# Optimization experiments

Hardware: AMD Instinct MI355X
Metric: run time of the kernel (lower is better)

## Reference

```python
import jax, jax.numpy as jnp
import numpy as np
from jax import lax

N_QUANTIZE = 256
N_AUX = 28
N_RESCH = 512
N_SKIPCH = 256
KS = 2
DILATIONS = [2 ** i for i in range(10)] * 3  # 30 layers
L = len(DILATIONS)


def _causal_conv(x, w, b, d):
    # x: (B, Cin, T), w: (Cout, Cin, KS) torch Conv1d layout, left-pad => causal
    pad = (w.shape[-1] - 1) * d
    y = lax.conv_general_dilated(x, w, window_strides=(1,), padding=[(pad, 0)],
                                 rhs_dilation=(d,),
                                 dimension_numbers=('NCH', 'OIH', 'NCH'))
    return y + b[None, :, None]


def _conv1x1(x, w, b):
    # x: (B, Cin, T), w: (Cout, Cin)
    return jnp.einsum('oi,bit->bot', w, x) + b[None, :, None]


def setup_inputs() -> dict:
    key = jax.random.key(0)
    ks = jax.random.split(key, 20)
    B, T = 2, 8000
    s = 0.05
    rn = lambda k, shape: (jax.random.normal(k, shape, jnp.float32) * s)
    inp = {
        'x': jax.random.randint(ks[0], (B, T), 0, N_QUANTIZE),
        'h': jax.random.normal(ks[1], (B, N_AUX, T), jnp.float32),
        'causal_w': rn(ks[2], (N_RESCH, N_QUANTIZE, KS)),
        'causal_b': rn(ks[3], (N_RESCH,)),
        'dil_sig_w': rn(ks[4], (L, N_RESCH, N_RESCH, KS)),
        'dil_sig_b': rn(ks[5], (L, N_RESCH)),
        'dil_tanh_w': rn(ks[6], (L, N_RESCH, N_RESCH, KS)),
        'dil_tanh_b': rn(ks[7], (L, N_RESCH)),
        'aux_sig_w': rn(ks[8], (L, N_RESCH, N_AUX)),
        'aux_sig_b': rn(ks[9], (L, N_RESCH)),
        'aux_tanh_w': rn(ks[10], (L, N_RESCH, N_AUX)),
        'aux_tanh_b': rn(ks[11], (L, N_RESCH)),
        'skip_w': rn(ks[12], (L, N_SKIPCH, N_RESCH)),
        'skip_b': rn(ks[13], (L, N_SKIPCH)),
        'res_w': rn(ks[14], (L, N_RESCH, N_RESCH)),
        'res_b': rn(ks[15], (L, N_RESCH)),
        'post1_w': rn(ks[16], (N_SKIPCH, N_SKIPCH)),
        'post1_b': rn(ks[17], (N_SKIPCH,)),
        'post2_w': rn(ks[18], (N_QUANTIZE, N_SKIPCH)),
        'post2_b': rn(ks[19], (N_QUANTIZE,)),
    }
    return inp


def reference(x, h, causal_w, causal_b, dil_sig_w, dil_sig_b, dil_tanh_w, dil_tanh_b,
              aux_sig_w, aux_sig_b, aux_tanh_w, aux_tanh_b, skip_w, skip_b,
              res_w, res_b, post1_w, post1_b, post2_w, post2_b):
    B, T = x.shape
    # _preprocess: onehot (B,T,Q) -> (B,Q,T), then causal conv
    oh = jax.nn.one_hot(x % N_QUANTIZE, N_QUANTIZE, dtype=jnp.float32).transpose(0, 2, 1)
    out = _causal_conv(oh, causal_w, causal_b, 1)  # (B, n_resch, T)
    skip_sum = jnp.zeros((B, N_SKIPCH, T), jnp.float32)
    for l, d in enumerate(DILATIONS):
        sig = _causal_conv(out, dil_sig_w[l], dil_sig_b[l], d) + _conv1x1(h, aux_sig_w[l], aux_sig_b[l])
        tan = _causal_conv(out, dil_tanh_w[l], dil_tanh_b[l], d) + _conv1x1(h, aux_tanh_w[l], aux_tanh_b[l])
        z = jax.nn.sigmoid(sig) * jnp.tanh(tan)
        skip_sum = skip_sum + _conv1x1(z, skip_w[l], skip_b[l])
        out = _conv1x1(z, res_w[l], res_b[l]) + out
    # _postprocess: relu -> 1x1 -> relu -> 1x1 -> (B, T, n_quantize)
    y = jax.nn.relu(skip_sum)
    y = jax.nn.relu(_conv1x1(y, post1_w, post1_b))
    y = _conv1x1(y, post2_w, post2_b)
    return y.transpose(0, 2, 1)
```

## Files before the change

kernel.cpp:

```cpp
#include <hip/hip_runtime.h>
#include <math.h>

#define T_LEN 8000
#define BATCH 2
#define CCH 512
#define SKP 256
#define AUXP 32
#define NQ 256
#define NLAYER 30
#define PADF 512
#define TPAD 8192
#define ROWS (PADF + TPAD)
#define HROWS TPAD

typedef unsigned short hfu;
typedef unsigned int u32;
typedef __attribute__((ext_vector_type(8))) _Float16 half8;
typedef __attribute__((ext_vector_type(4))) float f32x4;

#define GLOAD16(g, l)                                                          \
  __builtin_amdgcn_global_load_lds(                                            \
      (const __attribute__((address_space(1))) void*)(g),                      \
      (__attribute__((address_space(3))) void*)(l), 16, 0, 0)

__device__ inline hfu hfbits(float f) {
  union { _Float16 h; hfu u; } x;
  x.h = (_Float16)f;
  return x.u;
}
__device__ inline u32 pk2(float a, float b) {
  return (u32)hfbits(a) | ((u32)hfbits(b) << 16);
}
__device__ inline uint4 pk8(const float f[8]) {
  return make_uint4(pk2(f[0], f[1]), pk2(f[2], f[3]), pk2(f[4], f[5]), pk2(f[6], f[7]));
}
__device__ inline int ldsL(int row, int ck) {
  return ((row >> 1) << 3) + ((((ck) ^ ((row >> 1) & 3)) << 1) | (row & 1));
}

__global__ __launch_bounds__(256) void zero16(uint4* p, int n) {
  for (int i = blockIdx.x * 256 + threadIdx.x; i < n; i += gridDim.x * 256)
    p[i] = make_uint4(0u, 0u, 0u, 0u);
}

__global__ __launch_bounds__(256) void cvt_dil(const float* __restrict__ in, hfu* __restrict__ out) {
  const long NG = (long)NLAYER * CCH * (CCH / 4);
  for (long g = (long)blockIdx.x * 256 + threadIdx.x; g < NG; g += (long)gridDim.x * 256) {
    const int i4 = (int)(g & 127) * 4;
    const int o = (int)((g >> 7) & 511);
    const int l = (int)(g >> 16);
    const float* pp = in + (((size_t)l * CCH + o) * CCH + i4) * 2;
    float4 f0 = *(const float4*)pp;
    float4 f1 = *(const float4*)(pp + 4);
    uint2 t0 = make_uint2(pk2(f0.x, f0.z), pk2(f1.x, f1.z));
    uint2 t1 = make_uint2(pk2(f0.y, f0.w), pk2(f1.y, f1.w));
    hfu* ob = out + ((size_t)l * 2 * CCH + o) * CCH + i4;
    *(uint2*)ob = t0;
    *(uint2*)(ob + (size_t)CCH * CCH) = t1;
  }
}

__global__ __launch_bounds__(256) void cvt_skipres(const float* __restrict__ skw,
                                                   const float* __restrict__ rsw,
                                                   hfu* __restrict__ out) {
  const long NG = (long)NLAYER * 768 * (CCH / 4);
  for (long g = (long)blockIdx.x * 256 + threadIdx.x; g < NG; g += (long)gridDim.x * 256) {
    const int i4 = (int)(g & 127) * 4;
    const int r = (int)((g >> 7) % 768);
    const int l = (int)(g / (128 * 768));
    const float* src = (r < SKP) ? (skw + ((size_t)l * SKP + r) * CCH + i4)
                                 : (rsw + ((size_t)l * CCH + (r - SKP)) * CCH + i4);
    float4 f = *(const float4*)src;
    *(uint2*)(out + ((size_t)l * 768 + r) * CCH + i4) = make_uint2(pk2(f.x, f.y), pk2(f.z, f.w));
  }
}

__global__ __launch_bounds__(256) void cvt_aux(const float* __restrict__ in, hfu* __restrict__ out) {
  const int N = NLAYER * CCH * AUXP;
  for (int i = blockIdx.x * 256 + threadIdx.x; i < N; i += gridDim.x * 256) {
    const int j = i & 31;
    const int o = (i >> 5) & 511;
    const int l = i >> 14;
    float v = (j < 28) ? in[((size_t)l * CCH + o) * 28 + j] : 0.f;
    out[i] = hfbits(v);
  }
}

__global__ __launch_bounds__(256) void cvt_copy(const float* __restrict__ in, hfu* __restrict__ out, int n) {
  for (int i = blockIdx.x * 256 + threadIdx.x; i < n; i += gridDim.x * 256)
    out[i] = hfbits(in[i]);
}

__global__ __launch_bounds__(256) void cvt_cwt(const float* __restrict__ cw, float* __restrict__ out) {
  const int N = 2 * NQ * CCH;
  for (int i = blockIdx.x * 256 + threadIdx.x; i < N; i += gridDim.x * 256) {
    const int tap = i >> 17;
    const int r = i & 131071;
    const int xq = r >> 9;
    const int o = r & 511;
    out[i] = cw[((size_t)o * NQ + xq) * 2 + tap];
  }
}

__global__ __launch_bounds__(256) void htrans_kernel(const float* __restrict__ h, hfu* __restrict__ hbf) {
  const int b = blockIdx.y;
  const int t = blockIdx.x * 64 + (threadIdx.x & 63);
  const int j0 = threadIdx.x >> 6;
#pragma unroll
  for (int j = j0; j < AUXP; j += 4) {
    float v = (j < 28 && t < T_LEN) ? h[((size_t)b * 28 + j) * T_LEN + t] : 0.f;
    hbf[((size_t)b * HROWS + t) * AUXP + j] = hfbits(v);
  }
}

template <int PRE>
__global__ __launch_bounds__(256) void embed_kernel(const int* __restrict__ x,
                                                    const float* __restrict__ cwt,
                                                    const float* __restrict__ cb,
                                                    float* __restrict__ outf,
                                                    hfu* __restrict__ outb) {
  const int b = blockIdx.y;
  const int t = blockIdx.x * 4 + (threadIdx.x >> 6);
  const int o = (threadIdx.x & 63) * 8;
  const int xc = x[(size_t)b * T_LEN + t] & 255;
  const int xp = (t > 0) ? (x[(size_t)b * T_LEN + t - 1] & 255) : 0;
  const float won = (t > 0) ? 1.f : 0.f;
  const float* c1 = cwt + 131072 + (size_t)xc * CCH + o;
  const float* c0 = cwt + (size_t)xp * CCH + o;
  float v[8];
#pragma unroll
  for (int j = 0; j < 8; ++j) v[j] = cb[o + j] + c1[j] + won * c0[j];
  if (PRE) {
    *(uint4*)&outb[((size_t)b * ROWS + PADF + t) * CCH + o] = pk8(v);
  } else {
    float* po = outf + ((size_t)b * ROWS + PADF + t) * CCH + o;
    *(float4*)po = make_float4(v[0], v[1], v[2], v[3]);
    *(float4*)(po + 4) = make_float4(v[4], v[5], v[6], v[7]);
  }
}

template <int PRE>
__global__ __launch_bounds__(512, 2) void gate_kernel(
    const hfu* __restrict__ actb, const float* __restrict__ actf,
    const hfu* __restrict__ hbf,
    const void* __restrict__ wsp, const void* __restrict__ wtp,
    const hfu* __restrict__ auxs, const hfu* __restrict__ auxt,
    const float* __restrict__ bs1, const float* __restrict__ bs2,
    const float* __restrict__ bt1, const float* __restrict__ bt2,
    hfu* __restrict__ z, int d) {
  __shared__ uint4 sm[4096];
  const int tid = threadIdx.x;
  const int lane = tid & 63, wid = tid >> 6;
  const int wm = wid >> 2, wn = wid & 3;
  const int lr = lane & 15, lq = lane >> 4;

  const int n = blockIdx.x;
  const int f = (n & 7) * 32 + (n >> 3);
  const int tt = f >> 3, inner = f & 7;
  const int o0 = (inner >> 1) * 128;
  const int b = inner & 1;
  const int t0 = tt * 256;

  f32x4 accS[4][4] = {};
  f32x4 accT[4][4] = {};

  auto stage = [&](int ih, int p) {
    const int base = p * 2048;
    const int pr = tid >> 3, w = tid & 7;
    const int row = (pr << 1) | (w & 1);
    const int ck = (w >> 1) ^ (pr & 3);
    if (ih < 32) {
      const int tau = (ih < 16) ? 1 : 0;
      const int koff = (ih & 15) * 32;
      if (PRE) {
        const size_t wo = ((size_t)tau * CCH + o0 + row) * CCH + koff + ck * 8;
        GLOAD16((const hfu*)wsp + wo, &sm[base + tid]);
        GLOAD16((const hfu*)wtp + wo, &sm[base + 512 + tid]);
#pragma unroll
        for (int c = 0; c < 2; ++c) {
          const int s = c * 512 + tid;
          const int pr2 = s >> 3, w2 = s & 7;
          const int row2 = (pr2 << 1) | (w2 & 1);
          const int ck2 = (w2 >> 1) ^ (pr2 & 3);
          const hfu* ar = actb + ((size_t)b * ROWS + PADF + t0 + row2 - (tau ? 0 : d)) * CCH + koff + ck2 * 8;
          GLOAD16(ar, &sm[base + 1024 + s]);
        }
      } else {
        const float* wsf = (const float*)wsp;
        const float* wtf = (const float*)wtp;
        const size_t fb = ((size_t)(o0 + row) * CCH + koff + ck * 8) * 2;
        float vs[8], vt[8];
#pragma unroll
        for (int j = 0; j < 4; ++j) {
          float4 fs = *(const float4*)&wsf[fb + j * 4];
          float4 ft = *(const float4*)&wtf[fb + j * 4];
          vs[2 * j] = tau ? fs.y : fs.x;
          vs[2 * j + 1] = tau ? fs.w : fs.z;
          vt[2 * j] = tau ? ft.y : ft.x;
          vt[2 * j + 1] = tau ? ft.w : ft.z;
        }
        sm[base + tid] = pk8(vs);
        sm[base + 512 + tid] = pk8(vt);
#pragma unroll
        for (int c = 0; c < 2; ++c) {
          const int s = c * 512 + tid;
          const int pr2 = s >> 3, w2 = s & 7;
          const int row2 = (pr2 << 1) | (w2 & 1);
          const int ck2 = (w2 >> 1) ^ (pr2 & 3);
          const float* ar = actf + ((size_t)b * ROWS + PADF + t0 + row2 - (tau ? 0 : d)) * CCH + koff + ck2 * 8;
          float4 f0 = *(const float4*)&ar[0];
          float4 f1 = *(const float4*)&ar[4];
          float vb[8] = {f0.x, f0.y, f0.z, f0.w, f1.x, f1.y, f1.z, f1.w};
          sm[base + 1024 + s] = pk8(vb);
        }
      }
    } else {
      if (PRE) {
        GLOAD16(auxs + (size_t)(o0 + row) * AUXP + ck * 8, &sm[base + tid]);
        GLOAD16(auxt + (size_t)(o0 + row) * AUXP + ck * 8, &sm[base + 512 + tid]);
      } else {
        sm[base + tid] = *(const uint4*)&auxs[(size_t)(o0 + row) * AUXP + ck * 8];
        sm[base + 512 + tid] = *(const uint4*)&auxt[(size_t)(o0 + row) * AUXP + ck * 8];
      }
#pragma unroll
      for (int c = 0; c < 2; ++c) {
        const int s = c * 512 + tid;
        const int pr2 = s >> 3, w2 = s & 7;
        const int row2 = (pr2 << 1) | (w2 & 1);
        const int ck2 = (w2 >> 1) ^ (pr2 & 3);
        if (PRE)
          GLOAD16(hbf + ((size_t)b * HROWS + t0 + row2) * AUXP + ck2 * 8, &sm[base + 1024 + s]);
        else
          sm[base + 1024 + s] = *(const uint4*)&hbf[((size_t)b * HROWS + t0 + row2) * AUXP + ck2 * 8];
      }
    }
  };

  auto compute = [&](int p) {
    const int base = p * 2048;
    half8 af[4], ag[4], bv[4];
#pragma unroll
    for (int mr = 0; mr < 4; ++mr) {
      const int row = wm * 64 + mr * 16 + lr;
      const int idx = ldsL(row, lq);
      af[mr] = *(const half8*)&sm[base + idx];
      ag[mr] = *(const half8*)&sm[base + 512 + idx];
    }
#pragma unroll
    for (int nr = 0; nr < 4; ++nr) {
      const int row = wn * 64 + nr * 16 + lr;
      bv[nr] = *(const half8*)&sm[base + 1024 + ldsL(row, lq)];
    }
#pragma unroll
    for (int mr = 0; mr < 4; ++mr)
#pragma unroll
      for (int nr = 0; nr < 4; ++nr) {
        accS[mr][nr] = __builtin_amdgcn_mfma_f32_16x16x32_f16(af[mr], bv[nr], accS[mr][nr], 0, 0, 0);
        accT[mr][nr] = __builtin_amdgcn_mfma_f32_16x16x32_f16(ag[mr], bv[nr], accT[mr][nr], 0, 0, 0);
      }
  };

  if (PRE) {
    stage(0, 0);
    for (int ih = 0; ih < 33; ++ih) {
      if (ih < 32) {
        stage(ih + 1, (ih + 1) & 1);
        asm volatile("s_waitcnt vmcnt(4)" ::: "memory");
      } else {
        asm volatile("s_waitcnt vmcnt(0)" ::: "memory");
      }
      __builtin_amdgcn_s_barrier();
      __builtin_amdgcn_sched_barrier(0);
      __builtin_amdgcn_s_setprio(1);
      compute(ih & 1);
      __builtin_amdgcn_s_setprio(0);
      __builtin_amdgcn_sched_barrier(0);
      __builtin_amdgcn_s_barrier();
    }
  } else {
    for (int ih = 0; ih < 33; ++ih) {
      stage(ih, ih & 1);
      __syncthreads();
      compute(ih & 1);
      __syncthreads();
    }
  }

#pragma unroll
  for (int mr = 0; mr < 4; ++mr) {
    const int ob = o0 + wm * 64 + mr * 16 + lq * 4;
    float4 x1 = *(const float4*)&bs1[ob];
    float4 x2 = *(const float4*)&bs2[ob];
    float4 y1 = *(const float4*)&bt1[ob];
    float4 y2 = *(const float4*)&bt2[ob];
    const float sb[4] = {x1.x + x2.x, x1.y + x2.y, x1.z + x2.z, x1.w + x2.w};
    const float tb[4] = {y1.x + y2.x, y1.y + y2.y, y1.z + y2.z, y1.w + y2.w};
#pragma unroll
    for (int nr = 0; nr < 4; ++nr) {
      const int t = t0 + wn * 64 + nr * 16 + lr;
      float zv[4];
#pragma unroll
      for (int j = 0; j < 4; ++j) {
        float sv = accS[mr][nr][j] + sb[j];
        float tv = accT[mr][nr][j] + tb[j];
        float sg = __builtin_amdgcn_rcpf(1.f + __expf(-sv));
        float e2 = __expf(2.f * tv);
        float th = 1.f - 2.f * __builtin_amdgcn_rcpf(e2 + 1.f);
        zv[j] = sg * th;
      }
      *(uint2*)&z[((size_t)b * HROWS + t) * CCH + ob] = make_uint2(pk2(zv[0], zv[1]), pk2(zv[2], zv[3]));
    }
  }
}

template <int PRE>
__global__ __launch_bounds__(512, 4) void update_kernel(
    const hfu* __restrict__ z, const void* __restrict__ wp,
    const float* __restrict__ skwf, const float* __restrict__ rswf,
    const float* __restrict__ skb, const float* __restrict__ rsb,
    float* __restrict__ skip, float* __restrict__ outf, hfu* __restrict__ outb) {
  __shared__ uint4 sm[2048];
  const int tid = threadIdx.x;
  const int lane = tid & 63, wid = tid >> 6;
  const int wm = wid >> 1, wn = wid & 1;
  const int lr = lane & 15, lq = lane >> 4;

  const int n = blockIdx.x;
  const int xcd = n & 7, j = n >> 3;
  const int ttl = j / 12, inner = j % 12;
  const int tt = xcd * 8 + ttl;
  if (tt > 62) return;
  const int rg = inner >> 1, b = inner & 1;
  const int r0 = rg * 128;
  const int t0 = tt * 128;

  f32x4 acc[2][4] = {};

  auto stage_u = [&](int ih, int p) {
    const int base = p * 1024;
    const int pr = tid >> 3, w = tid & 7;
    const int row = (pr << 1) | (w & 1);
    const int ck = (w >> 1) ^ (pr & 3);
    const int k0 = ih * 32;
    if (PRE) {
      GLOAD16((const hfu*)wp + (size_t)(r0 + row) * CCH + k0 + ck * 8, &sm[base + tid]);
      GLOAD16(z + ((size_t)b * HROWS + t0 + row) * CCH + k0 + ck * 8, &sm[base + 512 + tid]);
    } else {
      const int R = r0 + row;
      const float* src = (R < SKP) ? (skwf + (size_t)R * CCH + k0 + ck * 8)
                                   : (rswf + (size_t)(R - SKP) * CCH + k0 + ck * 8);
      float4 f0 = *(const float4*)&src[0];
      float4 f1 = *(const float4*)&src[4];
      float v[8] = {f0.x, f0.y, f0.z, f0.w, f1.x, f1.y, f1.z, f1.w};
      sm[base + tid] = pk8(v);
      sm[base + 512 + tid] = *(const uint4*)&z[((size_t)b * HROWS + t0 + row) * CCH + k0 + ck * 8];
    }
  };

  auto compute_u = [&](int p) {
    const int base = p * 1024;
    half8 av[2], bv[4];
#pragma unroll
    for (int mr = 0; mr < 2; ++mr) {
      const int row = wm * 32 + mr * 16 + lr;
      av[mr] = *(const half8*)&sm[base + ldsL(row, lq)];
    }
#pragma unroll
    for (int nr = 0; nr < 4; ++nr) {
      const int row = wn * 64 + nr * 16 + lr;
      bv[nr] = *(const half8*)&sm[base + 512 + ldsL(row, lq)];
    }
#pragma unroll
    for (int mr = 0; mr < 2; ++mr)
#pragma unroll
      for (int nr = 0; nr < 4; ++nr)
        acc[mr][nr] = __builtin_amdgcn_mfma_f32_16x16x32_f16(av[mr], bv[nr], acc[mr][nr], 0, 0, 0);
  };

  if (PRE) {
    stage_u(0, 0);
    for (int ih = 0; ih < 16; ++ih) {
      if (ih < 15) {
        stage_u(ih + 1, (ih + 1) & 1);
        asm volatile("s_waitcnt vmcnt(2)" ::: "memory");
      } else {
        asm volatile("s_waitcnt vmcnt(0)" ::: "memory");
      }
      __builtin_amdgcn_s_barrier();
      __builtin_amdgcn_sched_barrier(0);
      __builtin_amdgcn_s_setprio(1);
      compute_u(ih & 1);
      __builtin_amdgcn_s_setprio(0);
      __builtin_amdgcn_sched_barrier(0);
      __builtin_amdgcn_s_barrier();
    }
  } else {
    for (int ih = 0; ih < 16; ++ih) {
      stage_u(ih, ih & 1);
      __syncthreads();
      compute_u(ih & 1);
      __syncthreads();
    }
  }

  const bool iskip = (r0 < SKP);
#pragma unroll
  for (int mr = 0; mr < 2; ++mr) {
    const int R = r0 + wm * 32 + mr * 16 + lq * 4;
#pragma unroll
    for (int nr = 0; nr < 4; ++nr) {
      const int t = t0 + wn * 64 + nr * 16 + lr;
      if (t < T_LEN) {
        if (iskip) {
          float4 bb = *(const float4*)&skb[R];
          float4* p = (float4*)&skip[((size_t)b * T_LEN + t) * SKP + R];
          float4 v = *p;
          v.x += acc[mr][nr][0] + bb.x;
          v.y += acc[mr][nr][1] + bb.y;
          v.z += acc[mr][nr][2] + bb.z;
          v.w += acc[mr][nr][3] + bb.w;
          *p = v;
        } else {
          const int rr = R - SKP;
          float4 bb = *(const float4*)&rsb[rr];
          if (PRE) {
            hfu* pb = &outb[((size_t)b * ROWS + PADF + t) * CCH + rr];
            uint2 old = *(uint2*)pb;
            const _Float16* hp = (const _Float16*)&old;
            float v0 = (float)hp[0] + acc[mr][nr][0] + bb.x;
            float v1 = (float)hp[1] + acc[mr][nr][1] + bb.y;
            float v2 = (float)hp[2] + acc[mr][nr][2] + bb.z;
            float v3 = (float)hp[3] + acc[mr][nr][3] + bb.w;
            *(uint2*)pb = make_uint2(pk2(v0, v1), pk2(v2, v3));
          } else {
            float4* p = (float4*)&outf[((size_t)b * ROWS + PADF + t) * CCH + rr];
            float4 v = *p;
            v.x += acc[mr][nr][0] + bb.x;
            v.y += acc[mr][nr][1] + bb.y;
            v.z += acc[mr][nr][2] + bb.z;
            v.w += acc[mr][nr][3] + bb.w;
            *p = v;
          }
        }
      }
    }
  }
}

__global__ __launch_bounds__(256, 2) void post1_kernel(const float* __restrict__ skip,
                                                       const hfu* __restrict__ w,
                                                       const float* __restrict__ bias,
                                                       hfu* __restrict__ y1) {
  __shared__ uint4 sm[2048];
  uint4* sA = sm;
  uint4* sB = sm + 1024;
  const int tid = threadIdx.x;
  const int lane = tid & 63, wid = tid >> 6;
  const int wm = wid >> 1, wn = wid & 1;
  const int lr = lane & 15, lq = lane >> 4;
  const int t0 = blockIdx.x * 128;
  const int r0 = blockIdx.y * 128;
  const int b = blockIdx.z;
  f32x4 acc[4][4] = {};
  for (int kt = 0; kt < 4; ++kt) {
#pragma unroll
    for (int c = 0; c < 4; ++c) {
      const int cb = c * 256 + wid * 64;
      const int ch = cb + lane;
      const int ksub = ch >> 7, mn = ch & 127;
      const int k0 = kt * 64 + ksub * 8;
      GLOAD16(w + (size_t)(r0 + mn) * SKP + k0, &sA[cb]);
      int row = t0 + mn;
      if (row > T_LEN - 1) row = T_LEN - 1;
      const float* src = skip + ((size_t)b * T_LEN + row) * SKP + k0;
      float4 f0 = *(const float4*)&src[0];
      float4 f1 = *(const float4*)&src[4];
      float v[8] = {fmaxf(f0.x, 0.f), fmaxf(f0.y, 0.f), fmaxf(f0.z, 0.f), fmaxf(f0.w, 0.f),
                    fmaxf(f1.x, 0.f), fmaxf(f1.y, 0.f), fmaxf(f1.z, 0.f), fmaxf(f1.w, 0.f)};
      sB[ch] = pk8(v);
    }
    __syncthreads();
#pragma unroll
    for (int ks = 0; ks < 2; ++ks) {
      const int kb = (ks * 4 + lq) * 128;
      half8 av[4], bv[4];
#pragma unroll
      for (int r = 0; r < 4; ++r) {
        av[r] = *(const half8*)&sA[kb + wm * 64 + r * 16 + lr];
        bv[r] = *(const half8*)&sB[kb + wn * 64 + r * 16 + lr];
      }
#pragma unroll
      for (int mr = 0; mr < 4; ++mr)
#pragma unroll
        for (int nr = 0; nr < 4; ++nr)
          acc[mr][nr] = __builtin_amdgcn_mfma_f32_16x16x32_f16(av[mr], bv[nr], acc[mr][nr], 0, 0, 0);
    }
    __syncthreads();
  }
#pragma unroll
  for (int mr = 0; mr < 4; ++mr) {
    const int ob = r0 + wm * 64 + mr * 16 + lq * 4;
    float4 bb = *(const float4*)&bias[ob];
    const float bs[4] = {bb.x, bb.y, bb.z, bb.w};
#pragma unroll
    for (int nr = 0; nr < 4; ++nr) {
      const int t = t0 + wn * 64 + nr * 16 + lr;
      float v[4];
#pragma unroll
      for (int j = 0; j < 4; ++j) v[j] = fmaxf(acc[mr][nr][j] + bs[j], 0.f);
      *(uint2*)&y1[((size_t)b * HROWS + t) * SKP + ob] = make_uint2(pk2(v[0], v[1]), pk2(v[2], v[3]));
    }
  }
}

__global__ __launch_bounds__(256, 2) void post2_kernel(const hfu* __restrict__ y1,
                                                       const hfu* __restrict__ w,
                                                       const float* __restrict__ bias,
                                                       float* __restrict__ outp) {
  __shared__ uint4 sm[2048];
  uint4* sA = sm;
  uint4* sB = sm + 1024;
  const int tid = threadIdx.x;
  const int lane = tid & 63, wid = tid >> 6;
  const int wm = wid >> 1, wn = wid & 1;
  const int lr = lane & 15, lq = lane >> 4;
  const int t0 = blockIdx.x * 128;
  const int r0 = blockIdx.y * 128;
  const int b = blockIdx.z;
  f32x4 acc[4][4] = {};
  for (int kt = 0; kt < 4; ++kt) {
#pragma unroll
    for (int c = 0; c < 4; ++c) {
      const int cb = c * 256 + wid * 64;
      const int ch = cb + lane;
      const int ksub = ch >> 7, mn = ch & 127;
      const int k0 = kt * 64 + ksub * 8;
      GLOAD16(w + (size_t)(r0 + mn) * SKP + k0, &sA[cb]);
      GLOAD16(y1 + ((size_t)b * HROWS + t0 + mn) * SKP + k0, &sB[cb]);
    }
    __syncthreads();
#pragma unroll
    for (int ks = 0; ks < 2; ++ks) {
      const int kb = (ks * 4 + lq) * 128;
      half8 av[4], bv[4];
#pragma unroll
      for (int r = 0; r < 4; ++r) {
        av[r] = *(const half8*)&sA[kb + wm * 64 + r * 16 + lr];
        bv[r] = *(const half8*)&sB[kb + wn * 64 + r * 16 + lr];
      }
#pragma unroll
      for (int mr = 0; mr < 4; ++mr)
#pragma unroll
        for (int nr = 0; nr < 4; ++nr)
          acc[mr][nr] = __builtin_amdgcn_mfma_f32_16x16x32_f16(av[mr], bv[nr], acc[mr][nr], 0, 0, 0);
    }
    __syncthreads();
  }
#pragma unroll
  for (int mr = 0; mr < 4; ++mr) {
    const int ob = r0 + wm * 64 + mr * 16 + lq * 4;
    float4 bb = *(const float4*)&bias[ob];
#pragma unroll
    for (int nr = 0; nr < 4; ++nr) {
      const int t = t0 + wn * 64 + nr * 16 + lr;
      if (t < T_LEN) {
        float4 v;
        v.x = acc[mr][nr][0] + bb.x;
        v.y = acc[mr][nr][1] + bb.y;
        v.z = acc[mr][nr][2] + bb.z;
        v.w = acc[mr][nr][3] + bb.w;
        *(float4*)&outp[((size_t)b * T_LEN + t) * NQ + ob] = v;
      }
    }
  }
}

extern "C" void kernel_launch(void* const* d_in, const int* in_sizes, int n_in,
                              void* d_out, int out_size, void* d_ws, size_t ws_size,
                              hipStream_t stream) {
  const int* x = (const int*)d_in[0];
  const float* h = (const float*)d_in[1];
  const float* causal_w = (const float*)d_in[2];
  const float* causal_b = (const float*)d_in[3];
  const float* dil_sig_w = (const float*)d_in[4];
  const float* dil_sig_b = (const float*)d_in[5];
  const float* dil_tanh_w = (const float*)d_in[6];
  const float* dil_tanh_b = (const float*)d_in[7];
  const float* aux_sig_w = (const float*)d_in[8];
  const float* aux_sig_b = (const float*)d_in[9];
  const float* aux_tanh_w = (const float*)d_in[10];
  const float* aux_tanh_b = (const float*)d_in[11];
  const float* skip_w = (const float*)d_in[12];
  const float* skip_b = (const float*)d_in[13];
  const float* res_w = (const float*)d_in[14];
  const float* res_b = (const float*)d_in[15];
  const float* post1_w = (const float*)d_in[16];
  const float* post1_b = (const float*)d_in[17];
  const float* post2_w = (const float*)d_in[18];
  const float* post2_b = (const float*)d_in[19];
  float* outp = (float*)d_out;

  char* p = (char*)d_ws;
  auto alloc = [&](size_t bytes) {
    char* r = p;
    p += (bytes + 255) & ~(size_t)255;
    return r;
  };
  float* outf = (float*)alloc((size_t)BATCH * ROWS * CCH * 4);
  float* skip = (float*)alloc((size_t)BATCH * T_LEN * SKP * 4);
  hfu* zb = (hfu*)alloc((size_t)BATCH * HROWS * CCH * 2);
  hfu* hbf = (hfu*)alloc((size_t)BATCH * HROWS * AUXP * 2);
  hfu* auxsb = (hfu*)alloc((size_t)NLAYER * CCH * AUXP * 2);
  hfu* auxtb = (hfu*)alloc((size_t)NLAYER * CCH * AUXP * 2);
  hfu* p1b = (hfu*)alloc((size_t)NQ * SKP * 2);
  hfu* p2b = (hfu*)alloc((size_t)NQ * SKP * 2);
  float* cwt = (float*)alloc((size_t)2 * NQ * CCH * 4);
  hfu* y1 = zb;
  hfu* outb = (hfu*)alloc((size_t)BATCH * ROWS * CCH * 2);
  hfu* dilS = (hfu*)alloc((size_t)NLAYER * 2 * CCH * CCH * 2);
  hfu* dilT = (hfu*)alloc((size_t)NLAYER * 2 * CCH * CCH * 2);
  hfu* wsr = (hfu*)alloc((size_t)NLAYER * 768 * CCH * 2);
  const bool pre = ((size_t)(p - (char*)d_ws) <= ws_size);

  cvt_aux<<<256, 256, 0, stream>>>(aux_sig_w, auxsb);
  cvt_aux<<<256, 256, 0, stream>>>(aux_tanh_w, auxtb);
  cvt_copy<<<64, 256, 0, stream>>>(post1_w, p1b, NQ * SKP);
  cvt_copy<<<64, 256, 0, stream>>>(post2_w, p2b, NQ * SKP);
  cvt_cwt<<<1024, 256, 0, stream>>>(causal_w, cwt);
  if (pre) {
    cvt_dil<<<2048, 256, 0, stream>>>(dil_sig_w, dilS);
    cvt_dil<<<2048, 256, 0, stream>>>(dil_tanh_w, dilT);
    cvt_skipres<<<2048, 256, 0, stream>>>(skip_w, res_w, wsr);
  }

  zero16<<<512, 256, 0, stream>>>((uint4*)skip, (int)((size_t)BATCH * T_LEN * SKP * 4 / 16));
  for (int b = 0; b < BATCH; ++b) {
    if (pre) {
      zero16<<<32, 256, 0, stream>>>((uint4*)(outb + (size_t)b * ROWS * CCH), PADF * CCH * 2 / 16);
      zero16<<<48, 256, 0, stream>>>((uint4*)(outb + ((size_t)b * ROWS + PADF + T_LEN) * CCH),
                                     (TPAD - T_LEN) * CCH * 2 / 16);
    } else {
      zero16<<<64, 256, 0, stream>>>((uint4*)(outf + (size_t)b * ROWS * CCH), PADF * CCH * 4 / 16);
      zero16<<<96, 256, 0, stream>>>((uint4*)(outf + ((size_t)b * ROWS + PADF + T_LEN) * CCH),
                                     (TPAD - T_LEN) * CCH * 4 / 16);
    }
  }

  htrans_kernel<<<dim3(128, 2), 256, 0, stream>>>(h, hbf);
  if (pre)
    embed_kernel<1><<<dim3(2000, 2), 256, 0, stream>>>(x, cwt, causal_b, nullptr, outb);
  else
    embed_kernel<0><<<dim3(2000, 2), 256, 0, stream>>>(x, cwt, causal_b, outf, nullptr);

  for (int l = 0; l < NLAYER; ++l) {
    const int d = 1 << (l % 10);
    if (pre) {
      gate_kernel<1><<<256, 512, 0, stream>>>(
          outb, nullptr, hbf, dilS + (size_t)l * 2 * CCH * CCH, dilT + (size_t)l * 2 * CCH * CCH,
          auxsb + (size_t)l * CCH * AUXP, auxtb + (size_t)l * CCH * AUXP,
          dil_sig_b + (size_t)l * CCH, aux_sig_b + (size_t)l * CCH,
          dil_tanh_b + (size_t)l * CCH, aux_tanh_b + (size_t)l * CCH, zb, d);
      update_kernel<1><<<768, 512, 0, stream>>>(
          zb, wsr + (size_t)l * 768 * CCH, nullptr, nullptr,
          skip_b + (size_t)l * SKP, res_b + (size_t)l * CCH, skip, nullptr, outb);
    } else {
      gate_kernel<0><<<256, 512, 0, stream>>>(
          nullptr, outf, hbf, dil_sig_w + (size_t)l * CCH * CCH * 2,
          dil_tanh_w + (size_t)l * CCH * CCH * 2,
          auxsb + (size_t)l * CCH * AUXP, auxtb + (size_t)l * CCH * AUXP,
          dil_sig_b + (size_t)l * CCH, aux_sig_b + (size_t)l * CCH,
          dil_tanh_b + (size_t)l * CCH, aux_tanh_b + (size_t)l * CCH, zb, d);
      update_kernel<0><<<768, 512, 0, stream>>>(
          zb, nullptr, skip_w + (size_t)l * SKP * CCH, res_w + (size_t)l * CCH * CCH,
          skip_b + (size_t)l * SKP, res_b + (size_t)l * CCH, skip, outf, nullptr);
    }
  }

  post1_kernel<<<dim3(63, 2, BATCH), 256, 0, stream>>>(skip, p1b, post1_b, y1);
  post2_kernel<<<dim3(63, 2, BATCH), 256, 0, stream>>>(y1, p2b, post2_b, outp);
}
```

Before: 2.166 ms.

## Halve gate tile height and use triple-buffered LDS pipeline in gate/update kernels

The gate kernel tile shrinks from 128 to 64 output channels, so the grid doubles to 512 blocks, accumulator registers halve, and launch bounds allow four blocks per CU. Both gate and update kernels move from a double-buffered to a triple-buffered LDS pipeline with prefetch distance two, dropping the trailing barrier per k-step. The aim is more parallelism and better latency hiding across 256 CUs. In exchange each activation tile is reloaded by twice as many blocks, adding global traffic, and LDS use per block grows.

```diff
diff --git a/kernel.cpp b/kernel.cpp
--- a/kernel.cpp
+++ b/kernel.cpp
@@ -140,7 +140,7 @@
 }
 
 template <int PRE>
-__global__ __launch_bounds__(512, 2) void gate_kernel(
+__global__ __launch_bounds__(512, 4) void gate_kernel(
     const hfu* __restrict__ actb, const float* __restrict__ actf,
     const hfu* __restrict__ hbf,
     const void* __restrict__ wsp, const void* __restrict__ wtp,
@@ -148,111 +148,105 @@
     const float* __restrict__ bs1, const float* __restrict__ bs2,
     const float* __restrict__ bt1, const float* __restrict__ bt2,
     hfu* __restrict__ z, int d) {
-  __shared__ uint4 sm[4096];
+  __shared__ uint4 sm[4608];
   const int tid = threadIdx.x;
   const int lane = tid & 63, wid = tid >> 6;
   const int wm = wid >> 2, wn = wid & 3;
   const int lr = lane & 15, lq = lane >> 4;
 
   const int n = blockIdx.x;
-  const int f = (n & 7) * 32 + (n >> 3);
-  const int tt = f >> 3, inner = f & 7;
-  const int o0 = (inner >> 1) * 128;
+  const int f = (n & 7) * 64 + (n >> 3);
+  const int tt = f >> 4, inner = f & 15;
+  const int o0 = (inner >> 1) * 64;
   const int b = inner & 1;
   const int t0 = tt * 256;
 
-  f32x4 accS[4][4] = {};
-  f32x4 accT[4][4] = {};
+  f32x4 accS[2][4] = {};
+  f32x4 accT[2][4] = {};
 
   auto stage = [&](int ih, int p) {
-    const int base = p * 2048;
-    const int pr = tid >> 3, w = tid & 7;
+    const int base = p * 1536;
+    const int s = tid & 255;
+    const int pr = s >> 3, w = s & 7;
     const int row = (pr << 1) | (w & 1);
     const int ck = (w >> 1) ^ (pr & 3);
     if (ih < 32) {
       const int tau = (ih < 16) ? 1 : 0;
       const int koff = (ih & 15) * 32;
       if (PRE) {
-        const size_t wo = ((size_t)tau * CCH + o0 + row) * CCH + koff + ck * 8;
-        GLOAD16((const hfu*)wsp + wo, &sm[base + tid]);
-        GLOAD16((const hfu*)wtp + wo, &sm[base + 512 + tid]);
+        const hfu* wsel = (tid < 256) ? (const hfu*)wsp : (const hfu*)wtp;
+        GLOAD16(wsel + ((size_t)tau * CCH + o0 + row) * CCH + koff + ck * 8, &sm[base + tid]);
 #pragma unroll
         for (int c = 0; c < 2; ++c) {
-          const int s = c * 512 + tid;
-          const int pr2 = s >> 3, w2 = s & 7;
+          const int s2 = c * 512 + tid;
+          const int pr2 = s2 >> 3, w2 = s2 & 7;
           const int row2 = (pr2 << 1) | (w2 & 1);
           const int ck2 = (w2 >> 1) ^ (pr2 & 3);
           const hfu* ar = actb + ((size_t)b * ROWS + PADF + t0 + row2 - (tau ? 0 : d)) * CCH + koff + ck2 * 8;
-          GLOAD16(ar, &sm[base + 1024 + s]);
+          GLOAD16(ar, &sm[base + 512 + s2]);
         }
       } else {
-        const float* wsf = (const float*)wsp;
-        const float* wtf = (const float*)wtp;
+        const float* wsel = (tid < 256) ? (const float*)wsp : (const float*)wtp;
         const size_t fb = ((size_t)(o0 + row) * CCH + koff + ck * 8) * 2;
-        float vs[8], vt[8];
+        float vs[8];
 #pragma unroll
         for (int j = 0; j < 4; ++j) {
-          float4 fs = *(const float4*)&wsf[fb + j * 4];
-          float4 ft = *(const float4*)&wtf[fb + j * 4];
+          float4 fs = *(const float4*)&wsel[fb + j * 4];
           vs[2 * j] = tau ? fs.y : fs.x;
           vs[2 * j + 1] = tau ? fs.w : fs.z;
-          vt[2 * j] = tau ? ft.y : ft.x;
-          vt[2 * j + 1] = tau ? ft.w : ft.z;
         }
         sm[base + tid] = pk8(vs);
-        sm[base + 512 + tid] = pk8(vt);
 #pragma unroll
         for (int c = 0; c < 2; ++c) {
-          const int s = c * 512 + tid;
-          const int pr2 = s >> 3, w2 = s & 7;
+          const int s2 = c * 512 + tid;
+          const int pr2 = s2 >> 3, w2 = s2 & 7;
           const int row2 = (pr2 << 1) | (w2 & 1);
           const int ck2 = (w2 >> 1) ^ (pr2 & 3);
           const float* ar = actf + ((size_t)b * ROWS + PADF + t0 + row2 - (tau ? 0 : d)) * CCH + koff + ck2 * 8;
           float4 f0 = *(const float4*)&ar[0];
           float4 f1 = *(const float4*)&ar[4];
           float vb[8] = {f0.x, f0.y, f0.z, f0.w, f1.x, f1.y, f1.z, f1.w};
-          sm[base + 1024 + s] = pk8(vb);
+          sm[base + 512 + s2] = pk8(vb);
         }
       }
     } else {
+      const hfu* asel = (tid < 256) ? auxs : auxt;
       if (PRE) {
-        GLOAD16(auxs + (size_t)(o0 + row) * AUXP + ck * 8, &sm[base + tid]);
-        GLOAD16(auxt + (size_t)(o0 + row) * AUXP + ck * 8, &sm[base + 512 + tid]);
+        GLOAD16(asel + (size_t)(o0 + row) * AUXP + ck * 8, &sm[base + tid]);
       } else {
-        sm[base + tid] = *(const uint4*)&auxs[(size_t)(o0 + row) * AUXP + ck * 8];
-        sm[base + 512 + tid] = *(const uint4*)&auxt[(size_t)(o0 + row) * AUXP + ck * 8];
+        sm[base + tid] = *(const uint4*)&asel[(size_t)(o0 + row) * AUXP + ck * 8];
       }
 #pragma unroll
       for (int c = 0; c < 2; ++c) {
-        const int s = c * 512 + tid;
-        const int pr2 = s >> 3, w2 = s & 7;
+        const int s2 = c * 512 + tid;
+        const int pr2 = s2 >> 3, w2 = s2 & 7;
         const int row2 = (pr2 << 1) | (w2 & 1);
         const int ck2 = (w2 >> 1) ^ (pr2 & 3);
         if (PRE)
-          GLOAD16(hbf + ((size_t)b * HROWS + t0 + row2) * AUXP + ck2 * 8, &sm[base + 1024 + s]);
+          GLOAD16(hbf + ((size_t)b * HROWS + t0 + row2) * AUXP + ck2 * 8, &sm[base + 512 + s2]);
         else
-          sm[base + 1024 + s] = *(const uint4*)&hbf[((size_t)b * HROWS + t0 + row2) * AUXP + ck2 * 8];
+          sm[base + 512 + s2] = *(const uint4*)&hbf[((size_t)b * HROWS + t0 + row2) * AUXP + ck2 * 8];
       }
     }
   };
 
   auto compute = [&](int p) {
-    const int base = p * 2048;
-    half8 af[4], ag[4], bv[4];
-#pragma unroll
-    for (int mr = 0; mr < 4; ++mr) {
-      const int row = wm * 64 + mr * 16 + lr;
+    const int base = p * 1536;
+    half8 af[2], ag[2], bv[4];
+#pragma unroll
+    for (int mr = 0; mr < 2; ++mr) {
+      const int row = wm * 32 + mr * 16 + lr;
       const int idx = ldsL(row, lq);
       af[mr] = *(const half8*)&sm[base + idx];
-      ag[mr] = *(const half8*)&sm[base + 512 + idx];
+      ag[mr] = *(const half8*)&sm[base + 256 + idx];
     }
 #pragma unroll
     for (int nr = 0; nr < 4; ++nr) {
       const int row = wn * 64 + nr * 16 + lr;
-      bv[nr] = *(const half8*)&sm[base + 1024 + ldsL(row, lq)];
-    }
-#pragma unroll
-    for (int mr = 0; mr < 4; ++mr)
+      bv[nr] = *(const half8*)&sm[base + 512 + ldsL(row, lq)];
+    }
+#pragma unroll
+    for (int mr = 0; mr < 2; ++mr)
 #pragma unroll
       for (int nr = 0; nr < 4; ++nr) {
         accS[mr][nr] = __builtin_amdgcn_mfma_f32_16x16x32_f16(af[mr], bv[nr], accS[mr][nr], 0, 0, 0);
@@ -262,33 +256,32 @@
 
   if (PRE) {
     stage(0, 0);
+    stage(1, 1);
     for (int ih = 0; ih < 33; ++ih) {
-      if (ih < 32) {
-        stage(ih + 1, (ih + 1) & 1);
-        asm volatile("s_waitcnt vmcnt(4)" ::: "memory");
-      } else {
+      if (ih < 32)
+        asm volatile("s_waitcnt vmcnt(3)" ::: "memory");
+      else
         asm volatile("s_waitcnt vmcnt(0)" ::: "memory");
-      }
       __builtin_amdgcn_s_barrier();
       __builtin_amdgcn_sched_barrier(0);
+      if (ih < 31) stage(ih + 2, (ih + 2) % 3);
       __builtin_amdgcn_s_setprio(1);
-      compute(ih & 1);
+      compute(ih % 3);
       __builtin_amdgcn_s_setprio(0);
       __builtin_amdgcn_sched_barrier(0);
-      __builtin_amdgcn_s_barrier();
     }
   } else {
     for (int ih = 0; ih < 33; ++ih) {
-      stage(ih, ih & 1);
+      stage(ih, ih % 3);
       __syncthreads();
-      compute(ih & 1);
+      compute(ih % 3);
       __syncthreads();
     }
   }
 
 #pragma unroll
-  for (int mr = 0; mr < 4; ++mr) {
-    const int ob = o0 + wm * 64 + mr * 16 + lq * 4;
+  for (int mr = 0; mr < 2; ++mr) {
+    const int ob = o0 + wm * 32 + mr * 16 + lq * 4;
     float4 x1 = *(const float4*)&bs1[ob];
     float4 x2 = *(const float4*)&bs2[ob];
     float4 y1 = *(const float4*)&bt1[ob];
@@ -319,7 +312,7 @@
     const float* __restrict__ skwf, const float* __restrict__ rswf,
     const float* __restrict__ skb, const float* __restrict__ rsb,
     float* __restrict__ skip, float* __restrict__ outf, hfu* __restrict__ outb) {
-  __shared__ uint4 sm[2048];
+  __shared__ uint4 sm[3072];
   const int tid = threadIdx.x;
   const int lane = tid & 63, wid = tid >> 6;
   const int wm = wid >> 1, wn = wid & 1;
@@ -379,26 +372,25 @@
 
   if (PRE) {
     stage_u(0, 0);
+    stage_u(1, 1);
     for (int ih = 0; ih < 16; ++ih) {
-      if (ih < 15) {
-        stage_u(ih + 1, (ih + 1) & 1);
+      if (ih < 15)
         asm volatile("s_waitcnt vmcnt(2)" ::: "memory");
-      } else {
+      else
         asm volatile("s_waitcnt vmcnt(0)" ::: "memory");
-      }
       __builtin_amdgcn_s_barrier();
       __builtin_amdgcn_sched_barrier(0);
+      if (ih < 14) stage_u(ih + 2, (ih + 2) % 3);
       __builtin_amdgcn_s_setprio(1);
-      compute_u(ih & 1);
+      compute_u(ih % 3);
       __builtin_amdgcn_s_setprio(0);
       __builtin_amdgcn_sched_barrier(0);
-      __builtin_amdgcn_s_barrier();
     }
   } else {
     for (int ih = 0; ih < 16; ++ih) {
-      stage_u(ih, ih & 1);
+      stage_u(ih, ih % 3);
       __syncthreads();
-      compute_u(ih & 1);
+      compute_u(ih % 3);
       __syncthreads();
     }
   }
@@ -655,7 +647,7 @@
   for (int l = 0; l < NLAYER; ++l) {
     const int d = 1 << (l % 10);
     if (pre) {
-      gate_kernel<1><<<256, 512, 0, stream>>>(
+      gate_kernel<1><<<512, 512, 0, stream>>>(
           outb, nullptr, hbf, dilS + (size_t)l * 2 * CCH * CCH, dilT + (size_t)l * 2 * CCH * CCH,
           auxsb + (size_t)l * CCH * AUXP, auxtb + (size_t)l * CCH * AUXP,
           dil_sig_b + (size_t)l * CCH, aux_sig_b + (size_t)l * CCH,
@@ -664,7 +656,7 @@
           zb, wsr + (size_t)l * 768 * CCH, nullptr, nullptr,
           skip_b + (size_t)l * SKP, res_b + (size_t)l * CCH, skip, nullptr, outb);
     } else {
-      gate_kernel<0><<<256, 512, 0, stream>>>(
+      gate_kernel<0><<<512, 512, 0, stream>>>(
           nullptr, outf, hbf, dil_sig_w + (size_t)l * CCH * CCH * 2,
           dil_tanh_w + (size_t)l * CCH * CCH * 2,
           auxsb + (size_t)l * CCH * AUXP, auxtb + (size_t)l * CCH * AUXP,
```

Result: no change. 2.205 ms (+1.8%).
